# Kernel optimization log

Measured on AMD Instinct MI355X. Metric: run time of the kernel, lower is better.

Reference implementation:

```python
import jax, jax.numpy as jnp
import numpy as np

B, L, D = 4, 4096, 1024  # batch, seq, d_model == in_features == out_features
E, R = 8, 8              # n_experts, r_base
DH = D // 2              # router hidden


def setup_inputs() -> dict:
    key = jax.random.key(0)
    ks = jax.random.split(key, 8)
    s = 0.02
    return {
        "x": jax.random.normal(ks[0], (B, L, D), dtype=jnp.float32),
        "W_base": jax.random.normal(ks[1], (D, D), dtype=jnp.float32) * s,
        "router_W1": jax.random.normal(ks[2], (DH, D), dtype=jnp.float32) * s,
        "router_b1": jnp.zeros((DH,), dtype=jnp.float32),
        "router_W2": jax.random.normal(ks[3], (E, DH), dtype=jnp.float32) * s,
        "router_b2": jnp.zeros((E,), dtype=jnp.float32),
        "temperature": jnp.asarray(1.0, dtype=jnp.float32),
        "lora_A": jax.random.normal(ks[4], (E, R, D), dtype=jnp.float32) * s,
        "lora_B": jax.random.normal(ks[5], (E, D, R), dtype=jnp.float32) * s,
    }


def reference(x, W_base, router_W1, router_b1, router_W2, router_b2,
              temperature, lora_A, lora_B):
    # Base frozen linear (bias=False): [B,L,D]
    base = jnp.einsum("bld,od->blo", x, W_base)
    # Router (eval mode: dropout inactive). hidden_states = x (Identity projection).
    h = jax.nn.relu(jnp.einsum("bld,hd->blh", x, router_W1) + router_b1)
    logits = (jnp.einsum("blh,eh->ble", h, router_W2) + router_b2) / temperature
    gates = jax.nn.softmax(logits, axis=-1)  # softmax over experts, [B,L,E]
    # All experts' low-rank projections batched: x @ A_e.T -> [B,L,E,R]
    xa = jnp.einsum("bld,erd->bler", x, lora_A)
    # Gate-weighted up-projection and sum over experts: [B,L,D]
    lora_out = jnp.einsum("bler,ble,edr->bld", xa, gates, lora_B)
    return base + lora_out
```

## Files before the change

kernel.cpp:

```cpp
#include <hip/hip_runtime.h>
#include <hip/hip_bf16.h>
#include <stdint.h>
#include <math.h>


#define M_TOK 16384

typedef unsigned short u16;
typedef short bf16x8 __attribute__((ext_vector_type(8)));
typedef float f32x4 __attribute__((ext_vector_type(4)));
typedef __attribute__((address_space(3))) uint32_t lds_u32_t;
typedef __attribute__((address_space(1))) const uint32_t glb_u32_t;

__device__ __forceinline__ u16 f2bf(float f) {
  uint32_t u = __builtin_bit_cast(uint32_t, f);
  return (u16)((u + 0x7fffu + ((u >> 16) & 1u)) >> 16);
}
__device__ __forceinline__ float bf2f(u16 v) {
  return __builtin_bit_cast(float, (uint32_t)v << 16);
}

__global__ __launch_bounds__(256) void prep_k(const float* __restrict__ x,
                                              const float* __restrict__ Wb,
                                              const float* __restrict__ rW1,
                                              const float* __restrict__ rW2,
                                              const float* __restrict__ loraA,
                                              const float* __restrict__ loraB,
                                              u16* __restrict__ xb,
                                              u16* __restrict__ Btb,
                                              u16* __restrict__ W1b,
                                              u16* __restrict__ W2b,
                                              u16* __restrict__ A2b) {
  const int g = blockIdx.x;
  const int tid = threadIdx.x;
  if (g < 16384) {
    int i = g * 256 + tid;
    float4 v = ((const float4*)x)[i];
    ushort4 o;
    o.x = f2bf(v.x); o.y = f2bf(v.y); o.z = f2bf(v.z); o.w = f2bf(v.w);
    ((ushort4*)xb)[i] = o;
  } else if (g < 17408) {
    int i = (g - 16384) * 256 + tid;
    int idx = i * 4;
    int row = idx >> 10, col = idx & 1023;
    float4 v = ((const float4*)Wb)[i];
    ushort4 o;
    o.x = f2bf(v.x); o.y = f2bf(v.y); o.z = f2bf(v.z); o.w = f2bf(v.w);
    *(ushort4*)(Btb + (size_t)row * 1088 + col) = o;
  } else if (g < 17920) {
    int i = (g - 17408) * 256 + tid;
    float4 v = ((const float4*)rW1)[i];
    ushort4 o;
    o.x = f2bf(v.x); o.y = f2bf(v.y); o.z = f2bf(v.z); o.w = f2bf(v.w);
    ((ushort4*)W1b)[i] = o;
  } else if (g < 18176) {
    int idx = (g - 17920) * 256 + tid;
    int n = idx >> 6, q = idx & 63;
    int e = q >> 3, r = q & 7;
    Btb[(size_t)n * 1088 + 1024 + q] = f2bf(loraB[((size_t)(e * 1024 + n)) * 8 + r]);
  } else if (g < 18240) {
    int i = (g - 18176) * 256 + tid;
    float4 v = ((const float4*)loraA)[i];
    ushort4 o;
    o.x = f2bf(v.x); o.y = f2bf(v.y); o.z = f2bf(v.z); o.w = f2bf(v.w);
    ((ushort4*)A2b)[i] = o;
  } else {
    int i = (g - 18240) * 256 + tid;
    int idx = i * 4;
    int row = idx >> 9, col = idx & 511;
    ushort4 o = {0, 0, 0, 0};
    if (row < 8) {
      float4 v = *(const float4*)(rW2 + (size_t)row * 512 + col);
      o.x = f2bf(v.x); o.y = f2bf(v.y); o.z = f2bf(v.z); o.w = f2bf(v.w);
    }
    ((ushort4*)W2b)[i] = o;
  }
}

__global__ __launch_bounds__(256) void gates2_k(const float* __restrict__ part,
                                                const float* __restrict__ b2,
                                                const float* __restrict__ temp,
                                                float* __restrict__ gates) {
  int m = blockIdx.x * 256 + threadIdx.x;
  float lg[8] = {};
#pragma unroll
  for (int q = 0; q < 4; ++q) {
    const float4* pp = (const float4*)(part + ((size_t)q * M_TOK + m) * 8);
    float4 a = pp[0], b = pp[1];
    lg[0] += a.x; lg[1] += a.y; lg[2] += a.z; lg[3] += a.w;
    lg[4] += b.x; lg[5] += b.y; lg[6] += b.z; lg[7] += b.w;
  }
  float t = temp[0], mx = -1e30f;
#pragma unroll
  for (int e = 0; e < 8; ++e) { lg[e] = (lg[e] + b2[e]) / t; mx = fmaxf(mx, lg[e]); }
  float s = 0.f;
#pragma unroll
  for (int e = 0; e < 8; ++e) { lg[e] = expf(lg[e] - mx); s += lg[e]; }
  float inv = 1.f / s;
  float* dst = gates + (size_t)m * 8;
  *(float4*)dst = make_float4(lg[0] * inv, lg[1] * inv, lg[2] * inv, lg[3] * inv);
  *((float4*)dst + 1) = make_float4(lg[4] * inv, lg[5] * inv, lg[6] * inv, lg[7] * inv);
}

template <int BM, int BN, int MODE>
__global__ __launch_bounds__(256) void gemm_mfma(const u16* __restrict__ A,
                                                 const u16* __restrict__ Bt,
                                                 const u16* __restrict__ A2,
                                                 void* __restrict__ Cv,
                                                 const float* __restrict__ aux,
                                                 int N, int K, int lda, int ldb) {
  constexpr int FM = BM / 32, FN = BN / 32;
  constexpr int AI = BM / 32, BI = BN / 32;
  __shared__ u16 lds[(BM + BN) * 64];
  u16* As = lds;
  u16* Bs = lds + BM * 64;

  const int tid = threadIdx.x;
  const int w = tid >> 6, lane = tid & 63;
  const int wr = w >> 1, wc = w & 1;
  const int m0 = blockIdx.y * BM, n0 = blockIdx.x * BN;

  const uint8_t* Ab = (const uint8_t*)A;
  const uint8_t* Bb = (const uint8_t*)Bt;
  const size_t lda_b = (size_t)lda * 2, ldb_b = (size_t)ldb * 2;

  f32x4 acc[FM][FN] = {};

  const int nk = K >> 6;
  for (int kt = 0; kt < nk; ++kt) {
#pragma unroll
    for (int i = 0; i < AI; ++i) {
      const int lbase = (w * AI + i) * 1024;
      const int o = lbase + lane * 16;
      const int r = o >> 7, cb = o & 127;
      const uint8_t* g = Ab + (size_t)(m0 + r) * lda_b + (size_t)kt * 128 + cb;
      __builtin_amdgcn_global_load_lds((glb_u32_t*)g,
                                       (lds_u32_t*)((uint8_t*)As + lbase), 16, 0, 0);
    }
#pragma unroll
    for (int i = 0; i < BI; ++i) {
      const int lbase = (w * BI + i) * 1024;
      const int o = lbase + lane * 16;
      const int r = o >> 7, cb = o & 127;
      const uint8_t* g = Bb + (size_t)(n0 + r) * ldb_b + (size_t)kt * 128 + cb;
      __builtin_amdgcn_global_load_lds((glb_u32_t*)g,
                                       (lds_u32_t*)((uint8_t*)Bs + lbase), 16, 0, 0);
    }
    __syncthreads();

    bf16x8 af[2][FM], bfv[2][FN];
#pragma unroll
    for (int ks = 0; ks < 2; ++ks) {
      const int col = ks * 32 + ((lane >> 4) << 3);
#pragma unroll
      for (int im = 0; im < FM; ++im) {
        const int row = wr * (BM / 2) + im * 16 + (lane & 15);
        af[ks][im] = *(const bf16x8*)(As + row * 64 + col);
      }
#pragma unroll
      for (int in_ = 0; in_ < FN; ++in_) {
        const int row = wc * (BN / 2) + in_ * 16 + (lane & 15);
        bfv[ks][in_] = *(const bf16x8*)(Bs + row * 64 + col);
      }
    }
#pragma unroll
    for (int ks = 0; ks < 2; ++ks)
#pragma unroll
      for (int im = 0; im < FM; ++im)
#pragma unroll
        for (int in_ = 0; in_ < FN; ++in_)
          acc[im][in_] = __builtin_amdgcn_mfma_f32_16x16x32_bf16(
              af[ks][im], bfv[ks][in_], acc[im][in_], 0, 0, 0);
    __syncthreads();
  }

#pragma unroll
  for (int im = 0; im < FM; ++im)
#pragma unroll
    for (int in_ = 0; in_ < FN; ++in_) {
      const int col = n0 + wc * (BN / 2) + in_ * 16 + (lane & 15);
#pragma unroll
      for (int j = 0; j < 4; ++j) {
        const int row = m0 + wr * (BM / 2) + im * 16 + ((lane >> 4) << 2) + j;
        float v = acc[im][in_][j];
        if constexpr (MODE == 1) {
          v *= aux[(size_t)row * 8 + (col >> 3)];
          ((u16*)Cv)[(size_t)row * N + col] = f2bf(v);
        } else {
          ((float*)Cv)[(size_t)row * N + col] = v;
        }
      }
    }
}

#define MFMA_Q(mh, nh)                                                         \
  _Pragma("unroll") for (int im2 = 0; im2 < FMH; ++im2)                        \
  _Pragma("unroll") for (int in2 = 0; in2 < FNH; ++in2)                        \
  _Pragma("unroll") for (int ks = 0; ks < 2; ++ks)                             \
      acc[(mh) * FMH + im2][(nh) * FNH + in2] =                                \
          __builtin_amdgcn_mfma_f32_16x16x32_bf16(                             \
              af[im2][ks], bfr[nh][in2][ks],                                   \
              acc[(mh) * FMH + im2][(nh) * FNH + in2], 0, 0, 0);

#define VMCNT(n) asm volatile("s_waitcnt vmcnt(%0)" ::"i"(n) : "memory")
#define BAR asm volatile("s_barrier" ::: "memory")
#define SP(x) __builtin_amdgcn_s_setprio(x)

template <int BM, int BN, int MODE>
__global__ __launch_bounds__(512, 2) void gemm8p(const u16* __restrict__ A,
                                                 const u16* __restrict__ Bt,
                                                 const u16* __restrict__ A2,
                                                 void* __restrict__ Cv,
                                                 const float* __restrict__ aux,
                                                 const int N, const int K,
                                                 const int lda, const int ldb) {
  constexpr int FM = BM / 32;
  constexpr int FNW = BN / 64;
  constexpr int FMH = FM / 2;
  constexpr int FNH = (FNW >= 2) ? FNW / 2 : 1;
  constexpr int NBH = BN / 128;
  constexpr int VMC = 2 * NBH;
  constexpr int BUFB = (BM + BN) * 128;

  __shared__ __align__(16) uint8_t lds[2 * BUFB];

  const int tid = threadIdx.x;
  const int lane = tid & 63, w = tid >> 6;
  const int wr = w >> 2, wcn = w & 3;
  const int l15 = lane & 15, lhi = lane >> 4;
  const int xorv = (lane & 7) << 4;
  const int c0 = (lhi * 16) ^ xorv;
  const int c1 = (64 + lhi * 16) ^ xorv;

  const int f = blockIdx.x;
  const int idx = (f & 7) * 32 + (f >> 3);
  const int gx = N / BN;
  const int m0 = (idx / gx) * BM;
  const int n0 = (idx % gx) * BN;

  const size_t lda_b = (size_t)lda * 2, ldb_b = (size_t)ldb * 2;
  const int nk = K >> 6;

  const int arow0 = (wr * (BM / 2) + l15) * 128;
  const int brow0 = (wcn * (BN / 4) + l15) * 128;

  f32x4 acc[FM][FNW] = {};
  bf16x8 af[FMH][2];
  bf16x8 bfr[2][FNH][2];

  auto stageA = [&](int h, int kt, int b) {
    const int ktc = kt < nk ? kt : nk - 1;
    const bool last = (MODE == 2) && (ktc == nk - 1);
    uint8_t* dst = lds + b * BUFB + h * (BM * 64) + w * 1024;
#pragma unroll
    for (int i = 0; i < 2; ++i) {
      const int off = i * 8192 + tid * 16;
      const int row = h * (BM / 2) + (off >> 7);
      const int ss = ((off >> 4) & 7) ^ (row & 7);
      const uint8_t* g =
          last ? (const uint8_t*)A2 + (size_t)(m0 + row) * 128 + ss * 16
               : (const uint8_t*)A + (size_t)(m0 + row) * lda_b + ktc * 128 + ss * 16;
      __builtin_amdgcn_global_load_lds((glb_u32_t*)g, (lds_u32_t*)(dst + i * 8192),
                                       16, 0, 0);
    }
  };
  auto stageB = [&](int h, int kt, int b) {
    const int ktc = kt < nk ? kt : nk - 1;
    uint8_t* dst = lds + b * BUFB + BM * 128 + h * (BN * 64) + w * 1024;
#pragma unroll
    for (int i = 0; i < 2; ++i) {
      const int off = i * 8192 + tid * 16;
      const int row = h * (BN / 2) + (off >> 7);
      const int ss = ((off >> 4) & 7) ^ (row & 7);
      const uint8_t* g =
          (const uint8_t*)Bt + (size_t)(n0 + row) * ldb_b + ktc * 128 + ss * 16;
      __builtin_amdgcn_global_load_lds((glb_u32_t*)g, (lds_u32_t*)(dst + i * 8192),
                                       16, 0, 0);
    }
  };

  auto loadA = [&](int mh, const uint8_t* buf) {
#pragma unroll
    for (int im2 = 0; im2 < FMH; ++im2) {
      const uint8_t* p = buf + arow0 + mh * (FMH * 2048) + im2 * 2048;
      af[im2][0] = *(const bf16x8*)(p + c0);
      af[im2][1] = *(const bf16x8*)(p + c1);
    }
  };
  auto loadB = [&](int nh, const uint8_t* buf) {
#pragma unroll
    for (int in2 = 0; in2 < FNH; ++in2) {
      const uint8_t* p = buf + BM * 128 + brow0 + nh * (FNH * 2048) + in2 * 2048;
      bfr[nh][in2][0] = *(const bf16x8*)(p + c0);
      bfr[nh][in2][1] = *(const bf16x8*)(p + c1);
    }
  };

  stageA(0, 0, 0); stageA(1, 0, 0);
  stageB(0, 0, 0); if constexpr (NBH == 2) stageB(1, 0, 0);
  stageB(0, 1, 1); if constexpr (NBH == 2) stageB(1, 1, 1);
  VMCNT(VMC); BAR;

  const uint8_t* b0 = lds;
  const uint8_t* b1 = lds + BUFB;
  const int NIT = nk >> 1;

  for (int it = 0; it < NIT; ++it) {
    const int u = it * 2;
    loadA(0, b0); loadB(0, b0);
    stageA(0, u + 1, 1);
    BAR; SP(1); MFMA_Q(0, 0); SP(0); BAR;
    loadB(1, b0);
    stageA(1, u + 1, 1);
    BAR; SP(1); MFMA_Q(0, 1); SP(0); BAR;
    loadA(1, b0);
    stageB(0, u + 2, 0);
    BAR; SP(1); MFMA_Q(1, 1); SP(0); BAR;
    if constexpr (NBH == 2) stageB(1, u + 2, 0);
    VMCNT(VMC);
    BAR; SP(1); MFMA_Q(1, 0); SP(0); BAR;
    loadA(0, b1); loadB(0, b1);
    stageA(0, u + 2, 0);
    BAR; SP(1); MFMA_Q(0, 0); SP(0); BAR;
    loadB(1, b1);
    stageA(1, u + 2, 0);
    BAR; SP(1); MFMA_Q(0, 1); SP(0); BAR;
    loadA(1, b1);
    stageB(0, u + 3, 1);
    BAR; SP(1); MFMA_Q(1, 1); SP(0); BAR;
    if constexpr (NBH == 2) stageB(1, u + 3, 1);
    VMCNT(VMC);
    BAR; SP(1); MFMA_Q(1, 0); SP(0); BAR;
  }

  if (nk & 1) {
    loadA(0, b0); loadB(0, b0);
    SP(1); MFMA_Q(0, 0); SP(0);
    loadB(1, b0);
    SP(1); MFMA_Q(0, 1); SP(0);
    loadA(1, b0);
    SP(1); MFMA_Q(1, 1); MFMA_Q(1, 0); SP(0);
  }

  if constexpr (MODE == 2) {
    float* C = (float*)Cv;
#pragma unroll
    for (int im = 0; im < FM; ++im) {
#pragma unroll
      for (int in_ = 0; in_ < FNW; ++in_) {
        const int col = n0 + wcn * (BN / 4) + in_ * 16 + l15;
#pragma unroll
        for (int j = 0; j < 4; ++j) {
          const int row = m0 + wr * (BM / 2) + im * 16 + lhi * 4 + j;
          C[(size_t)row * N + col] = acc[im][in_][j];
        }
      }
    }
  } else {
    u16* hs = (u16*)lds;
    __syncthreads();
#pragma unroll
    for (int im = 0; im < FM; ++im) {
#pragma unroll
      for (int in_ = 0; in_ < FNW; ++in_) {
        const int col = wcn * (BN / 4) + in_ * 16 + l15;
#pragma unroll
        for (int j = 0; j < 4; ++j) {
          const int row = wr * (BM / 2) + im * 16 + lhi * 4 + j;
          float v = fmaxf(acc[im][in_][j] + aux[n0 + col], 0.f);
          hs[row * 132 + col] = f2bf(v);
        }
      }
    }
    __syncthreads();
    const u16* w2b = (const u16*)A2;
    f32x4 acc2[2] = {};
#pragma unroll
    for (int ks = 0; ks < 4; ++ks) {
      bf16x8 bfrag = *(const bf16x8*)(w2b + (size_t)l15 * 512 + n0 + ks * 32 + lhi * 8);
#pragma unroll
      for (int im2 = 0; im2 < 2; ++im2) {
        const int mrow = w * 32 + im2 * 16 + l15;
        bf16x8 afrag = *(const bf16x8*)(hs + mrow * 132 + ks * 32 + lhi * 8);
        acc2[im2] = __builtin_amdgcn_mfma_f32_16x16x32_bf16(afrag, bfrag, acc2[im2],
                                                            0, 0, 0);
      }
    }
    if (l15 < 8) {
      float* part = (float*)Cv;
      const size_t base = (size_t)(n0 >> 7) * M_TOK;
#pragma unroll
      for (int im2 = 0; im2 < 2; ++im2)
#pragma unroll
        for (int j = 0; j < 4; ++j) {
          const int row = m0 + w * 32 + im2 * 16 + lhi * 4 + j;
          part[(base + row) * 8 + l15] = acc2[im2][j];
        }
    }
  }
}

extern "C" void kernel_launch(void* const* d_in, const int* in_sizes, int n_in,
                              void* d_out, int out_size, void* d_ws, size_t ws_size,
                              hipStream_t stream) {
  const float* x     = (const float*)d_in[0];
  const float* Wb    = (const float*)d_in[1];
  const float* rW1   = (const float*)d_in[2];
  const float* rb1   = (const float*)d_in[3];
  const float* rW2   = (const float*)d_in[4];
  const float* rb2   = (const float*)d_in[5];
  const float* temp  = (const float*)d_in[6];
  const float* loraA = (const float*)d_in[7];
  const float* loraB = (const float*)d_in[8];
  float* out = (float*)d_out;

  uint8_t* p = (uint8_t*)d_ws;
  u16* xb    = (u16*)p;   p += (size_t)M_TOK * 1024 * 2;
  u16* wb    = (u16*)p;   p += (size_t)M_TOK * 64 * 2;
  u16* Btb   = (u16*)p;   p += (size_t)1024 * 1088 * 2;
  u16* W1b   = (u16*)p;   p += (size_t)512 * 1024 * 2;
  u16* W2b   = (u16*)p;   p += (size_t)16 * 512 * 2;
  u16* A2b   = (u16*)p;   p += (size_t)64 * 1024 * 2;
  float* part  = (float*)p;  p += (size_t)4 * M_TOK * 8 * 4;
  float* gates = (float*)p;

  prep_k<<<18248, 256, 0, stream>>>(x, Wb, rW1, rW2, loraA, loraB,
                                    xb, Btb, W1b, W2b, A2b);

  gemm8p<256, 128, 3><<<256, 512, 0, stream>>>(xb, W1b, (const u16*)W2b, part,
                                               rb1, 512, 1024, 1024, 1024);

  gates2_k<<<M_TOK / 256, 256, 0, stream>>>(part, rb2, temp, gates);

  gemm_mfma<64, 64, 1><<<dim3(1, M_TOK / 64), 256, 0, stream>>>(
      xb, A2b, nullptr, wb, gates, 64, 1024, 1024, 1024);

  gemm8p<256, 256, 2><<<256, 512, 0, stream>>>(xb, Btb, wb, out, nullptr,
                                               1024, 1088, 1024, 1088);
}
```

Baseline: 97.91 us.

## Fuse gate softmax into LoRA-A GEMM and prefetch LDS fragments a phase ahead

```diff
diff --git a/kernel.cpp b/kernel.cpp
--- a/kernel.cpp
+++ b/kernel.cpp
@@ -77,63 +77,55 @@
   }
 }
 
-__global__ __launch_bounds__(256) void gates2_k(const float* __restrict__ part,
-                                                const float* __restrict__ b2,
-                                                const float* __restrict__ temp,
-                                                float* __restrict__ gates) {
-  int m = blockIdx.x * 256 + threadIdx.x;
-  float lg[8] = {};
-#pragma unroll
-  for (int q = 0; q < 4; ++q) {
-    const float4* pp = (const float4*)(part + ((size_t)q * M_TOK + m) * 8);
-    float4 a = pp[0], b = pp[1];
-    lg[0] += a.x; lg[1] += a.y; lg[2] += a.z; lg[3] += a.w;
-    lg[4] += b.x; lg[5] += b.y; lg[6] += b.z; lg[7] += b.w;
-  }
-  float t = temp[0], mx = -1e30f;
-#pragma unroll
-  for (int e = 0; e < 8; ++e) { lg[e] = (lg[e] + b2[e]) / t; mx = fmaxf(mx, lg[e]); }
-  float s = 0.f;
-#pragma unroll
-  for (int e = 0; e < 8; ++e) { lg[e] = expf(lg[e] - mx); s += lg[e]; }
-  float inv = 1.f / s;
-  float* dst = gates + (size_t)m * 8;
-  *(float4*)dst = make_float4(lg[0] * inv, lg[1] * inv, lg[2] * inv, lg[3] * inv);
-  *((float4*)dst + 1) = make_float4(lg[4] * inv, lg[5] * inv, lg[6] * inv, lg[7] * inv);
-}
-
-template <int BM, int BN, int MODE>
-__global__ __launch_bounds__(256) void gemm_mfma(const u16* __restrict__ A,
-                                                 const u16* __restrict__ Bt,
-                                                 const u16* __restrict__ A2,
-                                                 void* __restrict__ Cv,
-                                                 const float* __restrict__ aux,
-                                                 int N, int K, int lda, int ldb) {
-  constexpr int FM = BM / 32, FN = BN / 32;
-  constexpr int AI = BM / 32, BI = BN / 32;
+__global__ __launch_bounds__(256) void gemm_w(const u16* __restrict__ A,
+                                              const u16* __restrict__ Bt,
+                                              const float* __restrict__ part,
+                                              const float* __restrict__ b2,
+                                              const float* __restrict__ temp,
+                                              u16* __restrict__ Cv) {
+  constexpr int BM = 64, BN = 64, FM = 2, FN = 2, AI = 2, BI = 2;
   __shared__ u16 lds[(BM + BN) * 64];
+  __shared__ float g_lds[64][8];
   u16* As = lds;
   u16* Bs = lds + BM * 64;
 
   const int tid = threadIdx.x;
   const int w = tid >> 6, lane = tid & 63;
   const int wr = w >> 1, wc = w & 1;
-  const int m0 = blockIdx.y * BM, n0 = blockIdx.x * BN;
+  const int m0 = blockIdx.y * BM;
+
+  if (tid < 64) {
+    const int m = m0 + tid;
+    float lg[8] = {};
+#pragma unroll
+    for (int q = 0; q < 4; ++q) {
+      const float4* pp = (const float4*)(part + ((size_t)q * M_TOK + m) * 8);
+      float4 a = pp[0], b = pp[1];
+      lg[0] += a.x; lg[1] += a.y; lg[2] += a.z; lg[3] += a.w;
+      lg[4] += b.x; lg[5] += b.y; lg[6] += b.z; lg[7] += b.w;
+    }
+    float t = temp[0], mx = -1e30f;
+#pragma unroll
+    for (int e = 0; e < 8; ++e) { lg[e] = (lg[e] + b2[e]) / t; mx = fmaxf(mx, lg[e]); }
+    float s = 0.f;
+#pragma unroll
+    for (int e = 0; e < 8; ++e) { lg[e] = expf(lg[e] - mx); s += lg[e]; }
+    float inv = 1.f / s;
+#pragma unroll
+    for (int e = 0; e < 8; ++e) g_lds[tid][e] = lg[e] * inv;
+  }
 
   const uint8_t* Ab = (const uint8_t*)A;
   const uint8_t* Bb = (const uint8_t*)Bt;
-  const size_t lda_b = (size_t)lda * 2, ldb_b = (size_t)ldb * 2;
-
   f32x4 acc[FM][FN] = {};
 
-  const int nk = K >> 6;
-  for (int kt = 0; kt < nk; ++kt) {
+  for (int kt = 0; kt < 16; ++kt) {
 #pragma unroll
     for (int i = 0; i < AI; ++i) {
       const int lbase = (w * AI + i) * 1024;
       const int o = lbase + lane * 16;
       const int r = o >> 7, cb = o & 127;
-      const uint8_t* g = Ab + (size_t)(m0 + r) * lda_b + (size_t)kt * 128 + cb;
+      const uint8_t* g = Ab + (size_t)(m0 + r) * 2048 + (size_t)kt * 128 + cb;
       __builtin_amdgcn_global_load_lds((glb_u32_t*)g,
                                        (lds_u32_t*)((uint8_t*)As + lbase), 16, 0, 0);
     }
@@ -142,7 +134,7 @@
       const int lbase = (w * BI + i) * 1024;
       const int o = lbase + lane * 16;
       const int r = o >> 7, cb = o & 127;
-      const uint8_t* g = Bb + (size_t)(n0 + r) * ldb_b + (size_t)kt * 128 + cb;
+      const uint8_t* g = Bb + (size_t)r * 2048 + (size_t)kt * 128 + cb;
       __builtin_amdgcn_global_load_lds((glb_u32_t*)g,
                                        (lds_u32_t*)((uint8_t*)Bs + lbase), 16, 0, 0);
     }
@@ -154,12 +146,12 @@
       const int col = ks * 32 + ((lane >> 4) << 3);
 #pragma unroll
       for (int im = 0; im < FM; ++im) {
-        const int row = wr * (BM / 2) + im * 16 + (lane & 15);
+        const int row = wr * 32 + im * 16 + (lane & 15);
         af[ks][im] = *(const bf16x8*)(As + row * 64 + col);
       }
 #pragma unroll
       for (int in_ = 0; in_ < FN; ++in_) {
-        const int row = wc * (BN / 2) + in_ * 16 + (lane & 15);
+        const int row = wc * 32 + in_ * 16 + (lane & 15);
         bfv[ks][in_] = *(const bf16x8*)(Bs + row * 64 + col);
       }
     }
@@ -178,28 +170,23 @@
   for (int im = 0; im < FM; ++im)
 #pragma unroll
     for (int in_ = 0; in_ < FN; ++in_) {
-      const int col = n0 + wc * (BN / 2) + in_ * 16 + (lane & 15);
+      const int col = wc * 32 + in_ * 16 + (lane & 15);
 #pragma unroll
       for (int j = 0; j < 4; ++j) {
-        const int row = m0 + wr * (BM / 2) + im * 16 + ((lane >> 4) << 2) + j;
-        float v = acc[im][in_][j];
-        if constexpr (MODE == 1) {
-          v *= aux[(size_t)row * 8 + (col >> 3)];
-          ((u16*)Cv)[(size_t)row * N + col] = f2bf(v);
-        } else {
-          ((float*)Cv)[(size_t)row * N + col] = v;
-        }
-      }
-    }
-}
-
-#define MFMA_Q(mh, nh)                                                         \
+        const int lrow = wr * 32 + im * 16 + ((lane >> 4) << 2) + j;
+        float v = acc[im][in_][j] * g_lds[lrow][col >> 3];
+        Cv[(size_t)(m0 + lrow) * 64 + col] = f2bf(v);
+      }
+    }
+}
+
+#define MFMA_Q2(mh, nh, AF, BF)                                                \
   _Pragma("unroll") for (int im2 = 0; im2 < FMH; ++im2)                        \
   _Pragma("unroll") for (int in2 = 0; in2 < FNH; ++in2)                        \
   _Pragma("unroll") for (int ks = 0; ks < 2; ++ks)                             \
       acc[(mh) * FMH + im2][(nh) * FNH + in2] =                                \
           __builtin_amdgcn_mfma_f32_16x16x32_bf16(                             \
-              af[im2][ks], bfr[nh][in2][ks],                                   \
+              AF[im2][ks], BF[in2][ks],                                        \
               acc[(mh) * FMH + im2][(nh) * FNH + in2], 0, 0, 0);
 
 #define VMCNT(n) asm volatile("s_waitcnt vmcnt(%0)" ::"i"(n) : "memory")
@@ -207,7 +194,7 @@
 #define SP(x) __builtin_amdgcn_s_setprio(x)
 
 template <int BM, int BN, int MODE>
-__global__ __launch_bounds__(512, 2) void gemm8p(const u16* __restrict__ A,
+__global__ __launch_bounds__(512, 1) void gemm8p(const u16* __restrict__ A,
                                                  const u16* __restrict__ Bt,
                                                  const u16* __restrict__ A2,
                                                  void* __restrict__ Cv,
@@ -245,8 +232,8 @@
   const int brow0 = (wcn * (BN / 4) + l15) * 128;
 
   f32x4 acc[FM][FNW] = {};
-  bf16x8 af[FMH][2];
-  bf16x8 bfr[2][FNH][2];
+  bf16x8 A0f[FMH][2], A1f[FMH][2];
+  bf16x8 B0a[FNH][2], B0b[FNH][2], B1f[FNH][2];
 
   auto stageA = [&](int h, int kt, int b) {
     const int ktc = kt < nk ? kt : nk - 1;
@@ -279,67 +266,75 @@
     }
   };
 
-  auto loadA = [&](int mh, const uint8_t* buf) {
+  auto loadA = [&](int mh, const uint8_t* buf, bf16x8 (&dst)[FMH][2]) {
 #pragma unroll
     for (int im2 = 0; im2 < FMH; ++im2) {
       const uint8_t* p = buf + arow0 + mh * (FMH * 2048) + im2 * 2048;
-      af[im2][0] = *(const bf16x8*)(p + c0);
-      af[im2][1] = *(const bf16x8*)(p + c1);
+      dst[im2][0] = *(const bf16x8*)(p + c0);
+      dst[im2][1] = *(const bf16x8*)(p + c1);
     }
   };
-  auto loadB = [&](int nh, const uint8_t* buf) {
+  auto loadB = [&](int nh, const uint8_t* buf, bf16x8 (&dst)[FNH][2]) {
 #pragma unroll
     for (int in2 = 0; in2 < FNH; ++in2) {
       const uint8_t* p = buf + BM * 128 + brow0 + nh * (FNH * 2048) + in2 * 2048;
-      bfr[nh][in2][0] = *(const bf16x8*)(p + c0);
-      bfr[nh][in2][1] = *(const bf16x8*)(p + c1);
+      dst[in2][0] = *(const bf16x8*)(p + c0);
+      dst[in2][1] = *(const bf16x8*)(p + c1);
     }
   };
+
+  const uint8_t* b0 = lds;
+  const uint8_t* b1 = lds + BUFB;
 
   stageA(0, 0, 0); stageA(1, 0, 0);
   stageB(0, 0, 0); if constexpr (NBH == 2) stageB(1, 0, 0);
   stageB(0, 1, 1); if constexpr (NBH == 2) stageB(1, 1, 1);
   VMCNT(VMC); BAR;
-
-  const uint8_t* b0 = lds;
-  const uint8_t* b1 = lds + BUFB;
+  loadA(0, b0, A0f); loadB(0, b0, B0a);
+
   const int NIT = nk >> 1;
-
   for (int it = 0; it < NIT; ++it) {
-    const int u = it * 2;
-    loadA(0, b0); loadB(0, b0);
-    stageA(0, u + 1, 1);
-    BAR; SP(1); MFMA_Q(0, 0); SP(0); BAR;
-    loadB(1, b0);
-    stageA(1, u + 1, 1);
-    BAR; SP(1); MFMA_Q(0, 1); SP(0); BAR;
-    loadA(1, b0);
-    stageB(0, u + 2, 0);
-    BAR; SP(1); MFMA_Q(1, 1); SP(0); BAR;
-    if constexpr (NBH == 2) stageB(1, u + 2, 0);
+    const int t = it * 2;
+    stageA(0, t + 1, 1);
+    BAR;
+    loadB(1, b0, B1f);
+    SP(1); MFMA_Q2(0, 0, A0f, B0a); SP(0); BAR;
+    stageA(1, t + 1, 1);
+    BAR;
+    loadA(1, b0, A1f);
+    SP(1); MFMA_Q2(0, 1, A0f, B1f); SP(0); BAR;
+    stageB(0, t + 2, 0);
+    BAR;
+    SP(1); MFMA_Q2(1, 1, A1f, B1f); SP(0); BAR;
+    if constexpr (NBH == 2) stageB(1, t + 2, 0);
     VMCNT(VMC);
-    BAR; SP(1); MFMA_Q(1, 0); SP(0); BAR;
-    loadA(0, b1); loadB(0, b1);
-    stageA(0, u + 2, 0);
-    BAR; SP(1); MFMA_Q(0, 0); SP(0); BAR;
-    loadB(1, b1);
-    stageA(1, u + 2, 0);
-    BAR; SP(1); MFMA_Q(0, 1); SP(0); BAR;
-    loadA(1, b1);
-    stageB(0, u + 3, 1);
-    BAR; SP(1); MFMA_Q(1, 1); SP(0); BAR;
-    if constexpr (NBH == 2) stageB(1, u + 3, 1);
+    BAR;
+    loadA(0, b1, A0f); loadB(0, b1, B0b);
+    SP(1); MFMA_Q2(1, 0, A1f, B0a); SP(0); BAR;
+    stageA(0, t + 2, 0);
+    BAR;
+    loadB(1, b1, B1f);
+    SP(1); MFMA_Q2(0, 0, A0f, B0b); SP(0); BAR;
+    stageA(1, t + 2, 0);
+    BAR;
+    loadA(1, b1, A1f);
+    SP(1); MFMA_Q2(0, 1, A0f, B1f); SP(0); BAR;
+    stageB(0, t + 3, 1);
+    BAR;
+    SP(1); MFMA_Q2(1, 1, A1f, B1f); SP(0); BAR;
+    if constexpr (NBH == 2) stageB(1, t + 3, 1);
     VMCNT(VMC);
-    BAR; SP(1); MFMA_Q(1, 0); SP(0); BAR;
+    BAR;
+    loadA(0, b0, A0f); loadB(0, b0, B0a);
+    SP(1); MFMA_Q2(1, 0, A1f, B0b); SP(0); BAR;
   }
 
   if (nk & 1) {
-    loadA(0, b0); loadB(0, b0);
-    SP(1); MFMA_Q(0, 0); SP(0);
-    loadB(1, b0);
-    SP(1); MFMA_Q(0, 1); SP(0);
-    loadA(1, b0);
-    SP(1); MFMA_Q(1, 1); MFMA_Q(1, 0); SP(0);
+    loadB(1, b0, B1f);
+    SP(1); MFMA_Q2(0, 0, A0f, B0a); SP(0);
+    loadA(1, b0, A1f);
+    SP(1); MFMA_Q2(0, 1, A0f, B1f); SP(0);
+    SP(1); MFMA_Q2(1, 1, A1f, B1f); MFMA_Q2(1, 0, A1f, B0a); SP(0);
   }
 
   if constexpr (MODE == 2) {
@@ -421,8 +416,7 @@
   u16* W1b   = (u16*)p;   p += (size_t)512 * 1024 * 2;
   u16* W2b   = (u16*)p;   p += (size_t)16 * 512 * 2;
   u16* A2b   = (u16*)p;   p += (size_t)64 * 1024 * 2;
-  float* part  = (float*)p;  p += (size_t)4 * M_TOK * 8 * 4;
-  float* gates = (float*)p;
+  float* part = (float*)p;
 
   prep_k<<<18248, 256, 0, stream>>>(x, Wb, rW1, rW2, loraA, loraB,
                                     xb, Btb, W1b, W2b, A2b);
@@ -430,10 +424,7 @@
   gemm8p<256, 128, 3><<<256, 512, 0, stream>>>(xb, W1b, (const u16*)W2b, part,
                                                rb1, 512, 1024, 1024, 1024);
 
-  gates2_k<<<M_TOK / 256, 256, 0, stream>>>(part, rb2, temp, gates);
-
-  gemm_mfma<64, 64, 1><<<dim3(1, M_TOK / 64), 256, 0, stream>>>(
-      xb, A2b, nullptr, wb, gates, 64, 1024, 1024, 1024);
+  gemm_w<<<dim3(1, M_TOK / 64), 256, 0, stream>>>(xb, A2b, part, rb2, temp, wb);
 
   gemm8p<256, 256, 2><<<256, 512, 0, stream>>>(xb, Btb, wb, out, nullptr,
                                                1024, 1088, 1024, 1088);
```

Measured after the change: 114.5 us. 17.0% more time.
